# Optimization experiments

Measured on AMD Instinct MI355X. Metric: run time of the kernel, lower is better.

The kernel has to match this reference:

```python
import jax, jax.numpy as jnp
import numpy as np

D_MODEL = 128
NUM_HEADS = 4
D_HEAD = 32
ATTN_COEFF = 0.5
BATCH = 2
SEQ = 4096


def setup_inputs() -> dict:
    key = jax.random.key(0)
    k1, k2, k3, k4, k5 = jax.random.split(key, 5)
    std = 1.0 / np.sqrt(D_MODEL)
    x = jax.random.normal(k1, (BATCH, SEQ, D_MODEL), dtype=jnp.float32)
    W_K = jax.random.normal(k2, (NUM_HEADS, D_HEAD, D_MODEL), dtype=jnp.float32) * std
    W_Q = jax.random.normal(k3, (NUM_HEADS, D_HEAD, D_MODEL), dtype=jnp.float32) * std
    W_V = jax.random.normal(k4, (NUM_HEADS, D_HEAD, D_MODEL), dtype=jnp.float32) * std
    W_O = jax.random.normal(k5, (D_MODEL, NUM_HEADS * D_HEAD), dtype=jnp.float32) * std
    return {"x": x, "W_K": W_K, "W_Q": W_Q, "W_V": W_V, "W_O": W_O}


def reference(x, W_K, W_Q, W_V, W_O):
    batch, seq, _ = x.shape
    # projections: [B, H, S, Dh]
    k = jnp.einsum('ihd,bpd->biph', W_K, x)
    q = jnp.einsum('ihd,bpd->biph', W_Q, x)
    v = jnp.einsum('ihd,bpd->biph', W_V, x)
    # scores: [B, H, Sq, Sk]
    scores = jnp.einsum('biph,biqh->biqp', k, q) / np.sqrt(D_HEAD).astype(np.float32)
    # NOTE: original code builds a causal mask but never applies it; faithful omission.
    attn = jax.nn.softmax(scores, axis=-1)
    # post-softmax affine blend with uniform offset
    attn = attn * ATTN_COEFF + (1.0 - ATTN_COEFF)
    z = jnp.einsum('biph,biqp->biqh', v, attn)          # [B, H, S, Dh]
    z_flat = jnp.transpose(z, (0, 2, 1, 3)).reshape(batch, seq, NUM_HEADS * D_HEAD)
    out = jnp.einsum('df,bpf->bpd', W_O, z_flat)        # [B, S, D]
    return out
```

## Files before the change

kernel.cpp:

```cpp
#include <hip/hip_runtime.h>

#define SQ 4096
#define NB 2
#define NH 4
#define DH 32
#define DM 128

typedef float f32x16 __attribute__((ext_vector_type(16)));
typedef float f32x4  __attribute__((ext_vector_type(4)));
typedef __bf16 bf16x8 __attribute__((ext_vector_type(8)));
typedef unsigned int uint4v __attribute__((ext_vector_type(4)));
typedef unsigned short u16;

union B8 { uint4v u; bf16x8 b; };

__device__ inline u16 f2bf(float x) {
  unsigned u = __builtin_bit_cast(unsigned, x);
  unsigned r = (u + 0x7FFF + ((u >> 16) & 1)) >> 16;
  return (u16)r;
}

__device__ inline unsigned cvt_pk_bf16(float a, float b) {
  unsigned r;
  asm("v_cvt_pk_bf16_f32 %0, %1, %2" : "=v"(r) : "v"(a), "v"(b));
  return r;
}

__device__ inline void swap32(unsigned &a, unsigned &b) {
  asm("v_permlane32_swap_b32 %0, %1" : "+v"(a), "+v"(b));
}

#if __has_builtin(__builtin_amdgcn_exp2f)
#define EX2 __builtin_amdgcn_exp2f
#else
#define EX2 exp2f
#endif

__device__ inline float xhalf_max(float x) {
  unsigned ua = __builtin_bit_cast(unsigned, x), ub = ua;
  asm("v_permlane32_swap_b32 %0, %1" : "+v"(ua), "+v"(ub));
  return fmaxf(__builtin_bit_cast(float, ua), __builtin_bit_cast(float, ub));
}

__device__ inline float xhalf_add(float x) {
  unsigned ua = __builtin_bit_cast(unsigned, x), ub = ua;
  asm("v_permlane32_swap_b32 %0, %1" : "+v"(ua), "+v"(ub));
  return __builtin_bit_cast(float, ua) + __builtin_bit_cast(float, ub);
}

__device__ inline float tmax16(const f32x16& v) {
  float a0 = fmaxf(fmaxf(v[0], v[1]), v[2]);
  float a1 = fmaxf(fmaxf(v[3], v[4]), v[5]);
  float a2 = fmaxf(fmaxf(v[6], v[7]), v[8]);
  float a3 = fmaxf(fmaxf(v[9], v[10]), v[11]);
  float a4 = fmaxf(fmaxf(v[12], v[13]), v[14]);
  float b0 = fmaxf(fmaxf(a0, a1), a2);
  float b1 = fmaxf(fmaxf(a3, a4), v[15]);
  return fmaxf(b0, b1);
}

__global__ __launch_bounds__(256) void kprep(const float* __restrict__ x,
                                             const float* __restrict__ Wk,
                                             const float* __restrict__ Wq,
                                             const float* __restrict__ Wv,
                                             const float* __restrict__ Wo,
                                             u16* __restrict__ xb,
                                             u16* __restrict__ wb,
                                             float* __restrict__ xsum) {
  const int bid = blockIdx.x, t = threadIdx.x;
  if (bid < 256) {
    const size_t base = (size_t)bid * 4096 + (size_t)t * 16;
    const f32x4* src = (const f32x4*)(x + base);
    uint4v* dst = (uint4v*)(xb + base);
    f32x4 v0 = src[0], v1 = src[1], v2 = src[2], v3 = src[3];
    uint4v o0, o1;
    o0[0] = cvt_pk_bf16(v0[0], v0[1]); o0[1] = cvt_pk_bf16(v0[2], v0[3]);
    o0[2] = cvt_pk_bf16(v1[0], v1[1]); o0[3] = cvt_pk_bf16(v1[2], v1[3]);
    o1[0] = cvt_pk_bf16(v2[0], v2[1]); o1[1] = cvt_pk_bf16(v2[2], v2[3]);
    o1[2] = cvt_pk_bf16(v3[0], v3[1]); o1[3] = cvt_pk_bf16(v3[2], v3[3]);
    dst[0] = o0; dst[1] = o1;
  } else if (bid < 384) {
    const int j = bid - 256;
    const int b = j >> 6, rblk = j & 63;
    const int d = t & 127, rh = t >> 7;
    const float* xp = x + ((size_t)b * SQ + rblk * 64) * DM + d;
    float a = 0.f;
    for (int r = rh; r < 64; r += 2) a += xp[(size_t)r * DM];
    __shared__ float red[2][DM];
    red[rh][d] = a;
    __syncthreads();
    if (t < DM) atomicAdd(&xsum[b * DM + t], red[0][t] + red[1][t]);
  } else {
    const int m = bid - 384;
    if (m < 3) {
      const float* W = (m == 0) ? Wk : (m == 1 ? Wq : Wv);
      const float s = (m == 1) ? (1.4426950408889634f / 5.656854249492380f) : 1.0f;
      for (int i = t; i < DM * DM; i += 256) wb[m * DM * DM + i] = f2bf(W[i] * s);
    } else {
      for (int i = t; i < DM * DM; i += 256) wb[3 * DM * DM + i] = f2bf(Wo[i]);
    }
  }
}

__global__ __launch_bounds__(256) void kprojc(const u16* __restrict__ xb,
                                              const u16* __restrict__ wb,
                                              const float* __restrict__ Wv,
                                              const float* __restrict__ Wo,
                                              const float* __restrict__ xsum,
                                              u16* __restrict__ qb,
                                              u16* __restrict__ kb,
                                              u16* __restrict__ vt,
                                              float* __restrict__ cvec) {
  const int by = blockIdx.y;
  const int t = threadIdx.x;
  if (by == 12) {
    if (blockIdx.x >= NB) return;
    const int b = blockIdx.x;
    __shared__ float xs[DM], vs[DM];
    if (t < DM) xs[t] = xsum[b * DM + t];
    __syncthreads();
    const int c = t >> 1, half = t & 1;
    float a = 0.f;
    const float* wr = Wv + c * DM + half * 64;
    const float* xh = xs + half * 64;
    for (int i = 0; i < 64; ++i) a += wr[i] * xh[i];
    a += __shfl_xor(a, 1, 64);
    if (half == 0) vs[c] = a;
    __syncthreads();
    float a2 = 0.f;
    const float* wr2 = Wo + c * DM + half * 64;
    const float* vh = vs + half * 64;
    for (int i = 0; i < 64; ++i) a2 += wr2[i] * vh[i];
    a2 += __shfl_xor(a2, 1, 64);
    if (half == 0) cvec[b * DM + c] = 0.5f * a2;
    return;
  }
  const int lane = t & 63, wid = t >> 6;
  const int l31 = lane & 31, hi = lane >> 5;
  const int mat = by >> 2, h = by & 3;
  const int p0 = (blockIdx.x * 4 + wid) * 32;
  const u16* xrow = xb + (size_t)(p0 + l31) * DM + 8 * hi;
  const u16* wrow = wb + mat * DM * DM + (h * 32 + l31) * DM + 8 * hi;
  f32x16 acc;
#pragma unroll
  for (int r = 0; r < 16; ++r) acc[r] = 0.f;
#pragma unroll
  for (int ks = 0; ks < 8; ++ks) {
    B8 a, w;
    a.u = *(const uint4v*)(xrow + ks * 16);
    w.u = *(const uint4v*)(wrow + ks * 16);
    acc = __builtin_amdgcn_mfma_f32_32x32x16_bf16(a.b, w.b, acc, 0, 0, 0);
  }
  const int b = p0 >> 12, pl = p0 & (SQ - 1);
  const size_t bh = (size_t)b * NH + h;
  if (mat < 2) {
    u16* dst = (mat ? qb : kb) + (bh * SQ + pl) * DH + l31;
#pragma unroll
    for (int r = 0; r < 16; ++r) {
      int row = (r & 3) + 8 * (r >> 2) + 4 * hi;
      dst[(size_t)row * DH] = f2bf(acc[r]);
    }
  } else {
    u16* dst = vt + ((bh * (SQ / 32) + (pl >> 5)) * DH + l31) * 32;
#pragma unroll
    for (int r = 0; r < 16; ++r) {
      int row = (r & 3) + 8 * (r >> 2) + 4 * hi;
      dst[row] = f2bf(acc[r]);
    }
  }
}

#define TILE(K0, K1, V0, V1, NOFF) {                                               \
  f32x16 sc = __builtin_amdgcn_mfma_f32_32x32x16_bf16(K0.b, qf0.b, zacc, 0, 0, 0); \
  sc = __builtin_amdgcn_mfma_f32_32x32x16_bf16(K1.b, qf1.b, sc, 0, 0, 0);          \
  K0.u = *(const uint4v*)(kT + (NOFF));                                            \
  K1.u = *(const uint4v*)(kT + (NOFF) + 16);                                       \
  float pm = xhalf_max(tmax16(sc));                                                \
  if (__any(pm > m + 8.f)) {                                                       \
    float n = fmaxf(m, pm);                                                        \
    float rs = EX2(m - n);                                                         \
    s *= rs;                                                                       \
    _Pragma("unroll") for (int r = 0; r < 16; ++r) acc[r] *= rs;                   \
    m = n;                                                                         \
  }                                                                                \
  float p_[16];                                                                    \
  _Pragma("unroll") for (int r = 0; r < 16; ++r) p_[r] = EX2(sc[r] - m);           \
  float ls = ((p_[0]+p_[1])+(p_[2]+p_[3]))+((p_[4]+p_[5])+(p_[6]+p_[7]));          \
  ls += ((p_[8]+p_[9])+(p_[10]+p_[11]))+((p_[12]+p_[13])+(p_[14]+p_[15]));         \
  s += xhalf_add(ls);                                                              \
  unsigned w0 = cvt_pk_bf16(p_[0], p_[1]),  w1 = cvt_pk_bf16(p_[2], p_[3]);        \
  unsigned w2 = cvt_pk_bf16(p_[4], p_[5]),  w3 = cvt_pk_bf16(p_[6], p_[7]);        \
  unsigned w4 = cvt_pk_bf16(p_[8], p_[9]),  w5 = cvt_pk_bf16(p_[10], p_[11]);      \
  unsigned w6 = cvt_pk_bf16(p_[12], p_[13]), w7 = cvt_pk_bf16(p_[14], p_[15]);     \
  swap32(w0, w2); swap32(w1, w3); swap32(w4, w6); swap32(w5, w7);                  \
  B8 bp0_, bp1_;                                                                   \
  bp0_.u[0] = w0; bp0_.u[1] = w1; bp0_.u[2] = w2; bp0_.u[3] = w3;                  \
  bp1_.u[0] = w4; bp1_.u[1] = w5; bp1_.u[2] = w6; bp1_.u[3] = w7;                  \
  acc = __builtin_amdgcn_mfma_f32_32x32x16_bf16(V0.b, bp0_.b, acc, 0, 0, 0);       \
  acc = __builtin_amdgcn_mfma_f32_32x32x16_bf16(V1.b, bp1_.b, acc, 0, 0, 0);       \
  V0.u = *(const uint4v*)(vT + (NOFF));                                            \
  V1.u = *(const uint4v*)(vT + (NOFF) + 16);                                       \
}

__global__ __launch_bounds__(256, 4) void kattn(const u16* __restrict__ qb,
                                                const u16* __restrict__ kb,
                                                const u16* __restrict__ vt,
                                                u16* __restrict__ yb) {
  __shared__ float sm_[3][64], ss_[3][64], sa_[3][16][64];
  const int t = threadIdx.x, lane = t & 63, wid = t >> 6;
  const int l31 = lane & 31, hi = lane >> 5;
  const int bh = blockIdx.y;
  const int qbase = blockIdx.x * 32;

  const u16* qrow = qb + ((size_t)bh * SQ + qbase + l31) * DH + 8 * hi;
  B8 qf0, qf1;
  qf0.u = *(const uint4v*)(qrow);
  qf1.u = *(const uint4v*)(qrow + 16);

  const int kh = wid;
  const u16* kT = kb + ((size_t)bh * SQ + kh * 1024) * DH + l31 * 32 + 8 * hi;
  const u16* vT = vt + ((size_t)bh * (SQ / 32) + kh * 32) * (DH * 32) + l31 * 32 + 8 * hi;

  f32x16 zacc, acc;
#pragma unroll
  for (int r = 0; r < 16; ++r) { zacc[r] = 0.f; acc[r] = 0.f; }
  float m = -1e30f, s = 0.f;

  B8 ka0, ka1, va0, va1, kb0, kb1, vb0, vb1;
  ka0.u = *(const uint4v*)(kT);        ka1.u = *(const uint4v*)(kT + 16);
  va0.u = *(const uint4v*)(vT);        va1.u = *(const uint4v*)(vT + 16);
  kb0.u = *(const uint4v*)(kT + 1024); kb1.u = *(const uint4v*)(kT + 1024 + 16);
  vb0.u = *(const uint4v*)(vT + 1024); vb1.u = *(const uint4v*)(vT + 1024 + 16);

  for (int ti = 0; ti < 32; ti += 2) {
    const int off = ti << 10;
    TILE(ka0, ka1, va0, va1, off + 2048)
    TILE(kb0, kb1, vb0, vb1, off + 3072)
  }

  if (wid) {
    const int w = wid - 1;
    sm_[w][lane] = m;
    ss_[w][lane] = s;
#pragma unroll
    for (int r = 0; r < 16; ++r) sa_[w][r][lane] = acc[r];
  }
  __syncthreads();
  if (wid == 0) {
    float mm = m;
#pragma unroll
    for (int w = 0; w < 3; ++w) mm = fmaxf(mm, sm_[w][lane]);
    float e = EX2(m - mm);
    float den = s * e;
    float ew[3];
#pragma unroll
    for (int w = 0; w < 3; ++w) {
      ew[w] = EX2(sm_[w][lane] - mm);
      den += ss_[w][lane] * ew[w];
    }
    float inv = 0.5f / den;
    const int b = bh >> 2, h = bh & 3;
    u16* yp = yb + ((size_t)(b * SQ) + qbase + l31) * DM + h * 32;
#pragma unroll
    for (int r = 0; r < 16; ++r) {
      float o = acc[r] * e;
#pragma unroll
      for (int w = 0; w < 3; ++w) o += sa_[w][r][lane] * ew[w];
      int row = (r & 3) + 8 * (r >> 2) + 4 * hi;
      yp[row] = f2bf(o * inv);
    }
  }
}

__global__ __launch_bounds__(256) void kout(const u16* __restrict__ yb,
                                            const u16* __restrict__ wob,
                                            const float* __restrict__ cvec,
                                            float* __restrict__ out) {
  const int t = threadIdx.x, lane = t & 63, wid = t >> 6;
  const int l31 = lane & 31, hi = lane >> 5;
  const int blk = blockIdx.x;
  const int b = blk >> 7;
  const int p0 = (blk & 127) * 32;
  const int d0 = wid * 32;
  const u16* yrow = yb + ((size_t)(b * SQ) + p0 + l31) * DM + 8 * hi;
  const u16* wrow = wob + (size_t)(d0 + l31) * DM + 8 * hi;
  f32x16 acc;
#pragma unroll
  for (int r = 0; r < 16; ++r) acc[r] = 0.f;
#pragma unroll
  for (int ks = 0; ks < 8; ++ks) {
    B8 a, w;
    a.u = *(const uint4v*)(yrow + ks * 16);
    w.u = *(const uint4v*)(wrow + ks * 16);
    acc = __builtin_amdgcn_mfma_f32_32x32x16_bf16(a.b, w.b, acc, 0, 0, 0);
  }
  float cv = cvec[b * DM + d0 + l31];
  float* op = out + ((size_t)(b * SQ) + p0) * DM + d0 + l31;
#pragma unroll
  for (int r = 0; r < 16; ++r) {
    int row = (r & 3) + 8 * (r >> 2) + 4 * hi;
    op[(size_t)row * DM] = acc[r] + cv;
  }
}

extern "C" void kernel_launch(void* const* d_in, const int* in_sizes, int n_in,
                              void* d_out, int out_size, void* d_ws, size_t ws_size,
                              hipStream_t stream) {
  const float* x  = (const float*)d_in[0];
  const float* Wk = (const float*)d_in[1];
  const float* Wq = (const float*)d_in[2];
  const float* Wv = (const float*)d_in[3];
  const float* Wo = (const float*)d_in[4];
  float* out = (float*)d_out;
  char* ws = (char*)d_ws;
  float* xsum = (float*)(ws);
  float* cvec = (float*)(ws + (4 << 10));
  u16* wb = (u16*)(ws + (64 << 10));
  u16* qb = (u16*)(ws + (256 << 10));
  u16* kb = (u16*)(ws + (256 << 10) + ((size_t)2 << 20));
  u16* vt = (u16*)(ws + (256 << 10) + ((size_t)4 << 20));
  u16* yb = (u16*)(ws + (256 << 10) + ((size_t)6 << 20));
  u16* xb = yb;

  hipMemsetAsync(xsum, 0, NB * DM * sizeof(float), stream);
  kprep<<<dim3(388), dim3(256), 0, stream>>>(x, Wk, Wq, Wv, Wo, xb, wb, xsum);
  kprojc<<<dim3(64, 13), dim3(256), 0, stream>>>(xb, wb, Wv, Wo, xsum, qb, kb, vt, cvec);
  kattn<<<dim3(128, 8), dim3(256), 0, stream>>>(qb, kb, vt, yb);
  kout<<<dim3(256), dim3(256), 0, stream>>>(yb, wb + 3 * DM * DM, cvec, out);
}
```

Baseline: 124.3 us.

## Fuse bf16 conversion into projection, add MFMA priority hints, linearize attention grid

The projection kernel now reads fp32 x and weights directly and converts them to bf16 in registers, so the prep kernel no longer writes a bf16 copy of x or of Wk/Wq/Wv. The softmax scale for Q moves to the projection output. The attention kernel raises wave priority around its MFMA pairs, and its grid becomes 1-D with heads interleaved so blocks sharing a query tile land next to each other. The trade-off is that projection blocks re-read and re-convert fp32 data that several blocks share, which costs more load bandwidth per block.

```diff
diff --git a/kernel.cpp b/kernel.cpp
--- a/kernel.cpp
+++ b/kernel.cpp
@@ -59,29 +59,24 @@
   return fmaxf(b0, b1);
 }
 
+__device__ inline bf16x8 ld_cvt8(const float* p) {
+  f32x4 a = *(const f32x4*)p;
+  f32x4 b = *(const f32x4*)(p + 4);
+  B8 r;
+  r.u[0] = cvt_pk_bf16(a[0], a[1]);
+  r.u[1] = cvt_pk_bf16(a[2], a[3]);
+  r.u[2] = cvt_pk_bf16(b[0], b[1]);
+  r.u[3] = cvt_pk_bf16(b[2], b[3]);
+  return r.b;
+}
+
 __global__ __launch_bounds__(256) void kprep(const float* __restrict__ x,
-                                             const float* __restrict__ Wk,
-                                             const float* __restrict__ Wq,
-                                             const float* __restrict__ Wv,
                                              const float* __restrict__ Wo,
-                                             u16* __restrict__ xb,
-                                             u16* __restrict__ wb,
+                                             u16* __restrict__ wob,
                                              float* __restrict__ xsum) {
   const int bid = blockIdx.x, t = threadIdx.x;
-  if (bid < 256) {
-    const size_t base = (size_t)bid * 4096 + (size_t)t * 16;
-    const f32x4* src = (const f32x4*)(x + base);
-    uint4v* dst = (uint4v*)(xb + base);
-    f32x4 v0 = src[0], v1 = src[1], v2 = src[2], v3 = src[3];
-    uint4v o0, o1;
-    o0[0] = cvt_pk_bf16(v0[0], v0[1]); o0[1] = cvt_pk_bf16(v0[2], v0[3]);
-    o0[2] = cvt_pk_bf16(v1[0], v1[1]); o0[3] = cvt_pk_bf16(v1[2], v1[3]);
-    o1[0] = cvt_pk_bf16(v2[0], v2[1]); o1[1] = cvt_pk_bf16(v2[2], v2[3]);
-    o1[2] = cvt_pk_bf16(v3[0], v3[1]); o1[3] = cvt_pk_bf16(v3[2], v3[3]);
-    dst[0] = o0; dst[1] = o1;
-  } else if (bid < 384) {
-    const int j = bid - 256;
-    const int b = j >> 6, rblk = j & 63;
+  if (bid < 128) {
+    const int b = bid >> 6, rblk = bid & 63;
     const int d = t & 127, rh = t >> 7;
     const float* xp = x + ((size_t)b * SQ + rblk * 64) * DM + d;
     float a = 0.f;
@@ -91,19 +86,13 @@
     __syncthreads();
     if (t < DM) atomicAdd(&xsum[b * DM + t], red[0][t] + red[1][t]);
   } else {
-    const int m = bid - 384;
-    if (m < 3) {
-      const float* W = (m == 0) ? Wk : (m == 1 ? Wq : Wv);
-      const float s = (m == 1) ? (1.4426950408889634f / 5.656854249492380f) : 1.0f;
-      for (int i = t; i < DM * DM; i += 256) wb[m * DM * DM + i] = f2bf(W[i] * s);
-    } else {
-      for (int i = t; i < DM * DM; i += 256) wb[3 * DM * DM + i] = f2bf(Wo[i]);
-    }
-  }
-}
-
-__global__ __launch_bounds__(256) void kprojc(const u16* __restrict__ xb,
-                                              const u16* __restrict__ wb,
+    for (int i = t; i < DM * DM; i += 256) wob[i] = f2bf(Wo[i]);
+  }
+}
+
+__global__ __launch_bounds__(256) void kprojc(const float* __restrict__ x,
+                                              const float* __restrict__ Wk,
+                                              const float* __restrict__ Wq,
                                               const float* __restrict__ Wv,
                                               const float* __restrict__ Wo,
                                               const float* __restrict__ xsum,
@@ -139,27 +128,35 @@
   const int l31 = lane & 31, hi = lane >> 5;
   const int mat = by >> 2, h = by & 3;
   const int p0 = (blockIdx.x * 4 + wid) * 32;
-  const u16* xrow = xb + (size_t)(p0 + l31) * DM + 8 * hi;
-  const u16* wrow = wb + mat * DM * DM + (h * 32 + l31) * DM + 8 * hi;
+  const float* xrow = x + (size_t)(p0 + l31) * DM + 8 * hi;
+  const float* W = (mat == 0) ? Wk : (mat == 1 ? Wq : Wv);
+  const float* wrow = W + (h * 32 + l31) * DM + 8 * hi;
   f32x16 acc;
 #pragma unroll
   for (int r = 0; r < 16; ++r) acc[r] = 0.f;
 #pragma unroll
   for (int ks = 0; ks < 8; ++ks) {
-    B8 a, w;
-    a.u = *(const uint4v*)(xrow + ks * 16);
-    w.u = *(const uint4v*)(wrow + ks * 16);
-    acc = __builtin_amdgcn_mfma_f32_32x32x16_bf16(a.b, w.b, acc, 0, 0, 0);
-  }
+    bf16x8 af = ld_cvt8(xrow + ks * 16);
+    bf16x8 wf = ld_cvt8(wrow + ks * 16);
+    acc = __builtin_amdgcn_mfma_f32_32x32x16_bf16(af, wf, acc, 0, 0, 0);
+  }
+  const float QS = 1.4426950408889634f / 5.656854249492380f;
   const int b = p0 >> 12, pl = p0 & (SQ - 1);
   const size_t bh = (size_t)b * NH + h;
-  if (mat < 2) {
-    u16* dst = (mat ? qb : kb) + (bh * SQ + pl) * DH + l31;
+  if (mat == 0) {
+    u16* dst = kb + (bh * SQ + pl) * DH + l31;
 #pragma unroll
     for (int r = 0; r < 16; ++r) {
       int row = (r & 3) + 8 * (r >> 2) + 4 * hi;
       dst[(size_t)row * DH] = f2bf(acc[r]);
     }
+  } else if (mat == 1) {
+    u16* dst = qb + (bh * SQ + pl) * DH + l31;
+#pragma unroll
+    for (int r = 0; r < 16; ++r) {
+      int row = (r & 3) + 8 * (r >> 2) + 4 * hi;
+      dst[(size_t)row * DH] = f2bf(acc[r] * QS);
+    }
   } else {
     u16* dst = vt + ((bh * (SQ / 32) + (pl >> 5)) * DH + l31) * 32;
 #pragma unroll
@@ -171,8 +168,10 @@
 }
 
 #define TILE(K0, K1, V0, V1, NOFF) {                                               \
+  __builtin_amdgcn_s_setprio(1);                                                   \
   f32x16 sc = __builtin_amdgcn_mfma_f32_32x32x16_bf16(K0.b, qf0.b, zacc, 0, 0, 0); \
   sc = __builtin_amdgcn_mfma_f32_32x32x16_bf16(K1.b, qf1.b, sc, 0, 0, 0);          \
+  __builtin_amdgcn_s_setprio(0);                                                   \
   K0.u = *(const uint4v*)(kT + (NOFF));                                            \
   K1.u = *(const uint4v*)(kT + (NOFF) + 16);                                       \
   float pm = xhalf_max(tmax16(sc));                                                \
@@ -196,8 +195,10 @@
   B8 bp0_, bp1_;                                                                   \
   bp0_.u[0] = w0; bp0_.u[1] = w1; bp0_.u[2] = w2; bp0_.u[3] = w3;                  \
   bp1_.u[0] = w4; bp1_.u[1] = w5; bp1_.u[2] = w6; bp1_.u[3] = w7;                  \
+  __builtin_amdgcn_s_setprio(1);                                                   \
   acc = __builtin_amdgcn_mfma_f32_32x32x16_bf16(V0.b, bp0_.b, acc, 0, 0, 0);       \
   acc = __builtin_amdgcn_mfma_f32_32x32x16_bf16(V1.b, bp1_.b, acc, 0, 0, 0);       \
+  __builtin_amdgcn_s_setprio(0);                                                   \
   V0.u = *(const uint4v*)(vT + (NOFF));                                            \
   V1.u = *(const uint4v*)(vT + (NOFF) + 16);                                       \
 }
@@ -209,8 +210,8 @@
   __shared__ float sm_[3][64], ss_[3][64], sa_[3][16][64];
   const int t = threadIdx.x, lane = t & 63, wid = t >> 6;
   const int l31 = lane & 31, hi = lane >> 5;
-  const int bh = blockIdx.y;
-  const int qbase = blockIdx.x * 32;
+  const int bh = blockIdx.x & 7;
+  const int qbase = (blockIdx.x >> 3) * 32;
 
   const u16* qrow = qb + ((size_t)bh * SQ + qbase + l31) * DH + 8 * hi;
   B8 qf0, qf1;
@@ -315,16 +316,15 @@
   char* ws = (char*)d_ws;
   float* xsum = (float*)(ws);
   float* cvec = (float*)(ws + (4 << 10));
-  u16* wb = (u16*)(ws + (64 << 10));
+  u16* wob = (u16*)(ws + (64 << 10));
   u16* qb = (u16*)(ws + (256 << 10));
   u16* kb = (u16*)(ws + (256 << 10) + ((size_t)2 << 20));
   u16* vt = (u16*)(ws + (256 << 10) + ((size_t)4 << 20));
   u16* yb = (u16*)(ws + (256 << 10) + ((size_t)6 << 20));
-  u16* xb = yb;
 
   hipMemsetAsync(xsum, 0, NB * DM * sizeof(float), stream);
-  kprep<<<dim3(388), dim3(256), 0, stream>>>(x, Wk, Wq, Wv, Wo, xb, wb, xsum);
-  kprojc<<<dim3(64, 13), dim3(256), 0, stream>>>(xb, wb, Wv, Wo, xsum, qb, kb, vt, cvec);
-  kattn<<<dim3(128, 8), dim3(256), 0, stream>>>(qb, kb, vt, yb);
-  kout<<<dim3(256), dim3(256), 0, stream>>>(yb, wb + 3 * DM * DM, cvec, out);
-}
+  kprep<<<dim3(129), dim3(256), 0, stream>>>(x, Wo, wob, xsum);
+  kprojc<<<dim3(64, 13), dim3(256), 0, stream>>>(x, Wk, Wq, Wv, Wo, xsum, qb, kb, vt, cvec);
+  kattn<<<dim3(1024), dim3(256), 0, stream>>>(qb, kb, vt, yb);
+  kout<<<dim3(256), dim3(256), 0, stream>>>(yb, wob, cvec, out);
+}
```

Measured after the change: 128.6 us. 3.4% more time.
